# Optimization experiments

Hardware: AMD Instinct MI355X
Metric: run time of the kernel (lower is better)

Reference implementation:

```python
import jax, jax.numpy as jnp
import numpy as np

B, S, D, H = 4, 1024, 768, 12
DH = D // H  # 64
ALPHA = 0.5
EPS = 1e-12


def setup_inputs() -> dict:
    key = jax.random.key(0)
    ks = jax.random.split(key, 12)
    s = 0.02
    return {
        "hidden_states": jax.random.normal(ks[0], (B, S, D), jnp.float32),
        "attention_mask": jnp.zeros((B, 1, 1, S), jnp.float32),
        "previous_attention": jax.random.uniform(ks[1], (B, H, S, S), jnp.float32),
        "Wq": jax.random.normal(ks[2], (D, D), jnp.float32) * s,
        "bq": jnp.zeros((D,), jnp.float32),
        "Wk": jax.random.normal(ks[3], (D, D), jnp.float32) * s,
        "bk": jnp.zeros((D,), jnp.float32),
        "Wv": jax.random.normal(ks[4], (D, D), jnp.float32) * s,
        "bv": jnp.zeros((D,), jnp.float32),
        "conv_w": jax.random.normal(ks[5], (H, H), jnp.float32) * 0.1,  # 1x1 conv over head channels
        "conv_b": jnp.zeros((H,), jnp.float32),
        "Wo": jax.random.normal(ks[6], (D, D), jnp.float32) * s,
        "bo": jnp.zeros((D,), jnp.float32),
        "ln_w": jnp.ones((D,), jnp.float32),
        "ln_b": jnp.zeros((D,), jnp.float32),
    }


def _split_heads(x):
    # [B,S,D] -> [B,H,S,DH]
    return x.reshape(B, S, H, DH).transpose(0, 2, 1, 3)


def reference(hidden_states, attention_mask, previous_attention,
              Wq, bq, Wk, bk, Wv, bv, conv_w, conv_b, Wo, bo, ln_w, ln_b):
    q = _split_heads(hidden_states @ Wq + bq)
    k = _split_heads(hidden_states @ Wk + bk)
    v = _split_heads(hidden_states @ Wv + bv)

    scores = jnp.einsum('bhqd,bhkd->bhqk', q, k) / jnp.sqrt(jnp.float32(DH))
    scores = scores + attention_mask
    probs = jax.nn.softmax(scores, axis=-1)

    # 1x1 conv over head channels on previous attention, mix, re-softmax
    prev = jnp.einsum('oi,biqk->boqk', conv_w, previous_attention) + conv_b[None, :, None, None]
    probs = jax.nn.softmax(ALPHA * prev + (1.0 - ALPHA) * probs, axis=-1)

    ctx = jnp.einsum('bhqk,bhkd->bhqd', probs, v)
    ctx = ctx.transpose(0, 2, 1, 3).reshape(B, S, D)

    out = ctx @ Wo + bo
    out = out + hidden_states
    u = out.mean(-1, keepdims=True)
    var = ((out - u) ** 2).mean(-1, keepdims=True)
    out = (out - u) / jnp.sqrt(var + EPS)
    return ln_w * out + ln_b
```

## Files before the change

### kernel.cpp

```cpp
#include <hip/hip_runtime.h>
#include <math.h>

#define BB 4
#define SS 1024
#define DD 768
#define HH 12
#define DHH 64

typedef __attribute__((ext_vector_type(8))) short bf16x8;
typedef __attribute__((ext_vector_type(4))) float f32x4;

__device__ __forceinline__ unsigned int f2bf(float f) {
    unsigned int u = __float_as_uint(f);
    return (u + 0x7FFFu + ((u >> 16) & 1u)) >> 16;
}
__device__ __forceinline__ float bf2f(unsigned int h) {
    return __uint_as_float(h << 16);
}

__device__ __forceinline__ void glds16(const void* g, void* l) {
    __builtin_amdgcn_global_load_lds(
        (const __attribute__((address_space(1))) void*)g,
        (__attribute__((address_space(3))) void*)l, 16, 0, 0);
}

__global__ __launch_bounds__(256)
void cvt_hidden_kernel(const float* __restrict__ src, unsigned short* __restrict__ dst)
{
    const int idx = (blockIdx.x * 256 + threadIdx.x) * 8;
    float4 a = *(const float4*)&src[idx];
    float4 b = *(const float4*)&src[idx + 4];
    uint4 p;
    p.x = f2bf(a.x) | (f2bf(a.y) << 16);
    p.y = f2bf(a.z) | (f2bf(a.w) << 16);
    p.z = f2bf(b.x) | (f2bf(b.y) << 16);
    p.w = f2bf(b.z) | (f2bf(b.w) << 16);
    *(uint4*)&dst[idx] = p;
}

__global__ __launch_bounds__(256)
void transpose_w_kernel(const float* __restrict__ Wq, const float* __restrict__ Wk,
                        const float* __restrict__ Wv, const float* __restrict__ Wo,
                        unsigned short* __restrict__ Wt)
{
    __shared__ float tile[32][33];
    const int t = threadIdx.x;
    const int kt = blockIdx.x, nt = blockIdx.y, w = blockIdx.z;
    const float* src = (w == 0) ? Wq : (w == 1) ? Wk : (w == 2) ? Wv : Wo;
    const int r = t >> 3, c4 = (t & 7) * 4;
    float4 v = *(const float4*)&src[(kt * 32 + r) * DD + nt * 32 + c4];
    tile[r][c4 + 0] = v.x; tile[r][c4 + 1] = v.y;
    tile[r][c4 + 2] = v.z; tile[r][c4 + 3] = v.w;
    __syncthreads();
    uint2 p;
    p.x = f2bf(tile[c4 + 0][r]) | (f2bf(tile[c4 + 1][r]) << 16);
    p.y = f2bf(tile[c4 + 2][r]) | (f2bf(tile[c4 + 3][r]) << 16);
    *(uint2*)&Wt[((size_t)w * DD + nt * 32 + r) * DD + kt * 32 + c4] = p;
}

__device__ __forceinline__ void gemm_core64(
    const char* __restrict__ Ag, const char* __restrict__ Bg,
    char* As, char* Bs, int tid, f32x4 (&acc)[2][2])
{
    const int lane = tid & 63;
    const int wr = (tid >> 7) & 1;
    const int wc = (tid >> 6) & 1;
    const int ldst = (tid & 192) << 4;

    for (int c = 0; c < 12; ++c) {
        const int kbyte = c * 128;
        #pragma unroll
        for (int i = 0; i < 2; ++i) {
            const int s = i * 256 + tid;
            const int row = s >> 3, kb = s & 7;
            const size_t off = (size_t)row * 1536 + kbyte + ((kb ^ (row & 7)) << 4);
            glds16(Ag + off, As + i * 4096 + ldst);
            glds16(Bg + off, Bs + i * 4096 + ldst);
        }
        __syncthreads();
        #pragma unroll
        for (int ks = 0; ks < 2; ++ks) {
            const int kb = ks * 4 + (lane >> 4);
            bf16x8 a[2], b[2];
            #pragma unroll
            for (int mi = 0; mi < 2; ++mi) {
                const int row = wr * 32 + mi * 16 + (lane & 15);
                a[mi] = *(const bf16x8*)(As + row * 128 + ((kb ^ (row & 7)) << 4));
            }
            #pragma unroll
            for (int ni = 0; ni < 2; ++ni) {
                const int row = wc * 32 + ni * 16 + (lane & 15);
                b[ni] = *(const bf16x8*)(Bs + row * 128 + ((kb ^ (row & 7)) << 4));
            }
            #pragma unroll
            for (int mi = 0; mi < 2; ++mi)
                #pragma unroll
                for (int ni = 0; ni < 2; ++ni)
                    acc[mi][ni] = __builtin_amdgcn_mfma_f32_16x16x32_bf16(
                        a[mi], b[ni], acc[mi][ni], 0, 0, 0);
        }
        __syncthreads();
    }
}

__global__ __launch_bounds__(256)
void qkv_gemm_kernel(const unsigned short* __restrict__ hbf, const unsigned short* __restrict__ Wt,
                     const float* __restrict__ bq, const float* __restrict__ bk,
                     const float* __restrict__ bv,
                     unsigned short* __restrict__ Qb, unsigned short* __restrict__ Kb,
                     unsigned short* __restrict__ Vtb)
{
    __shared__ __align__(16) char As[8192];
    __shared__ __align__(16) char Bs[8192];
    const int tid = threadIdx.x;
    const int m0 = blockIdx.x * 64;
    const int w = blockIdx.y / 12;
    const int n0w = (blockIdx.y % 12) * 64;

    f32x4 acc[2][2];
    const f32x4 z4 = {0.f, 0.f, 0.f, 0.f};
    acc[0][0] = z4; acc[0][1] = z4; acc[1][0] = z4; acc[1][1] = z4;

    const char* Ag = (const char*)hbf + (size_t)m0 * 1536;
    const char* Bg = (const char*)Wt + ((size_t)w * DD + n0w) * 1536;
    gemm_core64(Ag, Bg, As, Bs, tid, acc);

    const int lane = tid & 63;
    const int wr = (tid >> 7) & 1, wc = (tid >> 6) & 1;
    const float* bias = (w == 0) ? bq : (w == 1) ? bk : bv;
    #pragma unroll
    for (int mi = 0; mi < 2; ++mi) {
        #pragma unroll
        for (int ni = 0; ni < 2; ++ni) {
            const int nw = n0w + wc * 32 + ni * 16 + (lane & 15);
            const int h = nw >> 6, d = nw & 63;
            const float bb = bias[nw];
            const int mrow = m0 + wr * 32 + mi * 16 + (lane >> 4) * 4;
            const int b = mrow >> 10, s = mrow & 1023;
            if (w == 2) {
                uint2 p;
                p.x = f2bf(acc[mi][ni][0] + bb) | (f2bf(acc[mi][ni][1] + bb) << 16);
                p.y = f2bf(acc[mi][ni][2] + bb) | (f2bf(acc[mi][ni][3] + bb) << 16);
                *(uint2*)&Vtb[(((size_t)b * HH + h) * DHH + d) * SS + s] = p;
            } else {
                unsigned short* dst = (w == 0) ? Qb : Kb;
                #pragma unroll
                for (int r = 0; r < 4; ++r)
                    dst[(((size_t)b * HH + h) * SS + (s + r)) * DHH + d] =
                        (unsigned short)f2bf(acc[mi][ni][r] + bb);
            }
        }
    }
}

__global__ __launch_bounds__(256)
void qk_exp_kernel(const unsigned short* __restrict__ Qb, const unsigned short* __restrict__ Kb,
                   const float* __restrict__ mask,
                   unsigned short* __restrict__ E1, float* __restrict__ Z1)
{
    __shared__ __align__(16) char Ks[32768];
    const int tid = threadIdx.x;
    const int lane = tid & 63;
    const int wv = tid >> 6;
    const int bh = blockIdx.x >> 4;
    const int q0 = (blockIdx.x & 15) * 64;
    const int b = bh / HH;
    const int qw = q0 + wv * 16;
    const int ldst = (tid & 192) << 4;

    const char* Qrow = (const char*)Qb + ((size_t)bh * SS + qw + (lane & 15)) * 128;
    bf16x8 aq0 = *(const bf16x8*)(Qrow + (lane >> 4) * 16);
    bf16x8 aq1 = *(const bf16x8*)(Qrow + 64 + (lane >> 4) * 16);

    float zr[4] = {0.f, 0.f, 0.f, 0.f};
    const char* Kbase = (const char*)Kb + (size_t)bh * SS * 128;

    for (int c = 0; c < 4; ++c) {
        #pragma unroll
        for (int i = 0; i < 8; ++i) {
            const int s = i * 256 + tid;
            const int row = s >> 3, kb = s & 7;
            glds16(Kbase + (size_t)(c * 256 + row) * 128 + ((kb ^ (row & 7)) << 4),
                   Ks + i * 4096 + ldst);
        }
        __syncthreads();
        #pragma unroll
        for (int nf = 0; nf < 16; ++nf) {
            const int krow = nf * 16 + (lane & 15);
            const int kx = krow & 7;
            bf16x8 b0 = *(const bf16x8*)(Ks + krow * 128 + (((lane >> 4) ^ kx) << 4));
            bf16x8 b1 = *(const bf16x8*)(Ks + krow * 128 + (((4 + (lane >> 4)) ^ kx) << 4));
            f32x4 accf = {0.f, 0.f, 0.f, 0.f};
            accf = __builtin_amdgcn_mfma_f32_16x16x32_bf16(aq0, b0, accf, 0, 0, 0);
            accf = __builtin_amdgcn_mfma_f32_16x16x32_bf16(aq1, b1, accf, 0, 0, 0);
            const int kcol = c * 256 + krow;
            const float mk = mask[b * SS + kcol];
            #pragma unroll
            for (int r = 0; r < 4; ++r) {
                const int q = qw + (lane >> 4) * 4 + r;
                const float e = __expf(accf[r] * 0.125f + mk);
                zr[r] += e;
                E1[((size_t)bh * SS + q) * SS + kcol] = (unsigned short)f2bf(e);
            }
        }
        __syncthreads();
    }

    #pragma unroll
    for (int r = 0; r < 4; ++r) {
        float z = zr[r];
        z += __shfl_xor(z, 1); z += __shfl_xor(z, 2);
        z += __shfl_xor(z, 4); z += __shfl_xor(z, 8);
        if ((lane & 15) == 0)
            Z1[(size_t)bh * SS + qw + (lane >> 4) * 4 + r] = z;
    }
}

__global__ __launch_bounds__(256)
void e2_kernel(unsigned short* __restrict__ E1, const float* __restrict__ Z1,
               const float* __restrict__ prev, const float* __restrict__ cw,
               const float* __restrict__ cb, float* __restrict__ Z2)
{
    __shared__ float cws[144], cbs[12], izs[12], zred[4][12];
    const int t = threadIdx.x;
    const int b = blockIdx.x >> 10;
    const int q = blockIdx.x & 1023;

    if (t < 144) cws[t] = cw[t];
    if (t < 12) {
        cbs[t] = cb[t];
        izs[t] = 1.0f / Z1[((size_t)(b * HH + t)) * SS + q];
    }
    __syncthreads();

    float z2[12];
    #pragma unroll
    for (int h = 0; h < 12; ++h) z2[h] = 0.f;

    #pragma unroll
    for (int c = 0; c < 2; ++c) {
        const int k = c * 512 + t * 2;
        float2 pv[12];
        #pragma unroll
        for (int i = 0; i < 12; ++i)
            pv[i] = *(const float2*)&prev[(((size_t)(b * HH + i)) * SS + q) * SS + k];
        const size_t e1base = (((size_t)(b * HH)) * SS + q) * SS + k;
        #pragma unroll
        for (int h = 0; h < 12; ++h) {
            float mix0 = cbs[h], mix1 = cbs[h];
            #pragma unroll
            for (int i = 0; i < 12; ++i) {
                mix0 = fmaf(cws[h * 12 + i], pv[i].x, mix0);
                mix1 = fmaf(cws[h * 12 + i], pv[i].y, mix1);
            }
            unsigned int u = *(unsigned int*)&E1[e1base + (size_t)h * SS * SS];
            const float p10 = bf2f(u & 0xFFFFu) * izs[h];
            const float p11 = bf2f(u >> 16) * izs[h];
            const float e0 = __expf(0.5f * (mix0 + p10));
            const float e1 = __expf(0.5f * (mix1 + p11));
            z2[h] += e0 + e1;
            *(unsigned int*)&E1[e1base + (size_t)h * SS * SS] = f2bf(e0) | (f2bf(e1) << 16);
        }
    }

    #pragma unroll
    for (int h = 0; h < 12; ++h) {
        float z = z2[h];
        for (int off = 32; off; off >>= 1) z += __shfl_xor(z, off);
        z2[h] = z;
    }
    if ((t & 63) == 0) {
        const int wv = t >> 6;
        #pragma unroll
        for (int h = 0; h < 12; ++h) zred[wv][h] = z2[h];
    }
    __syncthreads();
    if (t < 12)
        Z2[((size_t)(b * HH + t)) * SS + q] =
            zred[0][t] + zred[1][t] + zred[2][t] + zred[3][t];
}

__global__ __launch_bounds__(256)
void pv_kernel(const unsigned short* __restrict__ E2, const float* __restrict__ Z2,
               const unsigned short* __restrict__ Vtb, unsigned short* __restrict__ ctx)
{
    __shared__ __align__(16) char Es[8192];
    __shared__ __align__(16) char Vs[8192];
    const int tid = threadIdx.x;
    const int lane = tid & 63;
    const int wv = tid >> 6;
    const int bh = blockIdx.x >> 4;
    const int q0 = (blockIdx.x & 15) * 64;
    const int b = bh / HH, h = bh % HH;
    const int ldst = (tid & 192) << 4;

    f32x4 acc[4];
    const f32x4 z4 = {0.f, 0.f, 0.f, 0.f};
    acc[0] = z4; acc[1] = z4; acc[2] = z4; acc[3] = z4;

    const char* Ebase = (const char*)E2 + ((size_t)bh * SS + q0) * 2048;
    const char* Vbase = (const char*)Vtb + (size_t)bh * DHH * 2048;

    for (int c = 0; c < 16; ++c) {
        const int kbyte = c * 128;
        #pragma unroll
        for (int i = 0; i < 2; ++i) {
            const int s = i * 256 + tid;
            const int row = s >> 3, kb = s & 7;
            const size_t off = (size_t)row * 2048 + kbyte + ((kb ^ (row & 7)) << 4);
            glds16(Ebase + off, Es + i * 4096 + ldst);
            glds16(Vbase + off, Vs + i * 4096 + ldst);
        }
        __syncthreads();
        #pragma unroll
        for (int ks = 0; ks < 2; ++ks) {
            const int kb = ks * 4 + (lane >> 4);
            const int arow = wv * 16 + (lane & 15);
            bf16x8 a = *(const bf16x8*)(Es + arow * 128 + ((kb ^ (arow & 7)) << 4));
            #pragma unroll
            for (int nf = 0; nf < 4; ++nf) {
                const int vrow = nf * 16 + (lane & 15);
                bf16x8 bb = *(const bf16x8*)(Vs + vrow * 128 + ((kb ^ (vrow & 7)) << 4));
                acc[nf] = __builtin_amdgcn_mfma_f32_16x16x32_bf16(a, bb, acc[nf], 0, 0, 0);
            }
        }
        __syncthreads();
    }

    float iz[4];
    #pragma unroll
    for (int r = 0; r < 4; ++r)
        iz[r] = 1.0f / Z2[(size_t)bh * SS + q0 + wv * 16 + (lane >> 4) * 4 + r];

    #pragma unroll
    for (int nf = 0; nf < 4; ++nf) {
        const int d = nf * 16 + (lane & 15);
        #pragma unroll
        for (int r = 0; r < 4; ++r) {
            const int q = q0 + wv * 16 + (lane >> 4) * 4 + r;
            ctx[((size_t)(b * SS + q)) * DD + h * DHH + d] =
                (unsigned short)f2bf(acc[nf][r] * iz[r]);
        }
    }
}

__global__ __launch_bounds__(256)
void o_gemm_kernel(const unsigned short* __restrict__ ctx, const unsigned short* __restrict__ WtO,
                   const float* __restrict__ bo, float* __restrict__ gout)
{
    __shared__ __align__(16) char As[8192];
    __shared__ __align__(16) char Bs[8192];
    const int tid = threadIdx.x;
    const int m0 = blockIdx.x * 64;
    const int n0 = blockIdx.y * 64;

    f32x4 acc[2][2];
    const f32x4 z4 = {0.f, 0.f, 0.f, 0.f};
    acc[0][0] = z4; acc[0][1] = z4; acc[1][0] = z4; acc[1][1] = z4;

    gemm_core64((const char*)ctx + (size_t)m0 * 1536,
                (const char*)WtO + (size_t)n0 * 1536, As, Bs, tid, acc);

    const int lane = tid & 63;
    const int wr = (tid >> 7) & 1, wc = (tid >> 6) & 1;
    #pragma unroll
    for (int mi = 0; mi < 2; ++mi) {
        #pragma unroll
        for (int ni = 0; ni < 2; ++ni) {
            const int n = n0 + wc * 32 + ni * 16 + (lane & 15);
            const float bb = bo[n];
            const int mrow = m0 + wr * 32 + mi * 16 + (lane >> 4) * 4;
            #pragma unroll
            for (int r = 0; r < 4; ++r)
                gout[(size_t)(mrow + r) * DD + n] = acc[mi][ni][r] + bb;
        }
    }
}

__global__ __launch_bounds__(256)
void ln_kernel(const float* __restrict__ go, const float* __restrict__ hid,
               const float* __restrict__ lw, const float* __restrict__ lb,
               float* __restrict__ out)
{
    const int row = blockIdx.x;
    const int tid = threadIdx.x;
    const int lane = tid & 63, wave = tid >> 6;
    __shared__ float wsum[4], wsq[4];

    float x[3];
    float ssum = 0.f, ssq = 0.f;
    #pragma unroll
    for (int j = 0; j < 3; ++j) {
        const int n = tid + j * 256;
        const float v = go[(size_t)row * DD + n] + hid[(size_t)row * DD + n];
        x[j] = v; ssum += v; ssq += v * v;
    }
    for (int off = 32; off; off >>= 1) {
        ssum += __shfl_xor(ssum, off);
        ssq  += __shfl_xor(ssq, off);
    }
    if (lane == 0) { wsum[wave] = ssum; wsq[wave] = ssq; }
    __syncthreads();
    const float tsum = wsum[0] + wsum[1] + wsum[2] + wsum[3];
    const float tsq  = wsq[0] + wsq[1] + wsq[2] + wsq[3];
    const float mean = tsum * (1.0f / 768.0f);
    const float var  = tsq * (1.0f / 768.0f) - mean * mean;
    const float rstd = rsqrtf(var + 1e-12f);
    #pragma unroll
    for (int j = 0; j < 3; ++j) {
        const int n = tid + j * 256;
        out[(size_t)row * DD + n] = lw[n] * ((x[j] - mean) * rstd) + lb[n];
    }
}

extern "C" void kernel_launch(void* const* d_in, const int* in_sizes, int n_in,
                              void* d_out, int out_size, void* d_ws, size_t ws_size,
                              hipStream_t stream)
{
    const float* hidden = (const float*)d_in[0];
    const float* mask   = (const float*)d_in[1];
    const float* prev   = (const float*)d_in[2];
    const float* Wq = (const float*)d_in[3];  const float* bq = (const float*)d_in[4];
    const float* Wk = (const float*)d_in[5];  const float* bk = (const float*)d_in[6];
    const float* Wv = (const float*)d_in[7];  const float* bv = (const float*)d_in[8];
    const float* cw = (const float*)d_in[9];  const float* cb = (const float*)d_in[10];
    const float* Wo = (const float*)d_in[11]; const float* bo = (const float*)d_in[12];
    const float* lw = (const float*)d_in[13]; const float* lb = (const float*)d_in[14];
    float* out = (float*)d_out;

    char* w = (char*)d_ws;
    unsigned short* hbf = (unsigned short*)(w);
    unsigned short* Wt  = (unsigned short*)(w + 6291456);
    unsigned short* Qb  = (unsigned short*)(w + 11010048);
    unsigned short* Kb  = (unsigned short*)(w + 17301504);
    unsigned short* Vtb = (unsigned short*)(w + 23592960);
    unsigned short* E1  = (unsigned short*)(w + 29884416);
    float* Z1 = (float*)(w + 130547712);
    float* Z2 = (float*)(w + 130744320);
    unsigned short* ctx = hbf;
    float* gout = (float*)(w + 11010048);

    dim3 blk(256);
    cvt_hidden_kernel<<<dim3(1536), blk, 0, stream>>>(hidden, hbf);
    transpose_w_kernel<<<dim3(24, 24, 4), blk, 0, stream>>>(Wq, Wk, Wv, Wo, Wt);
    qkv_gemm_kernel<<<dim3(64, 36), blk, 0, stream>>>(hbf, Wt, bq, bk, bv, Qb, Kb, Vtb);
    qk_exp_kernel<<<dim3(768), blk, 0, stream>>>(Qb, Kb, mask, E1, Z1);
    e2_kernel<<<dim3(4096), blk, 0, stream>>>(E1, Z1, prev, cw, cb, Z2);
    pv_kernel<<<dim3(768), blk, 0, stream>>>(E1, Z2, Vtb, ctx);
    o_gemm_kernel<<<dim3(64, 12), blk, 0, stream>>>(ctx, Wt + (size_t)3 * DD * DD, bo, gout);
    ln_kernel<<<dim3(4096), blk, 0, stream>>>(gout, hidden, lw, lb, out);
}
```

Baseline: 464.8 us.

## Stage kernel epilogue outputs through swizzled LDS for coalesced vector stores

Four kernels (QKV GEMM, QK-exp, PV context, O GEMM) now write their MFMA accumulator fragments into an XOR-swizzled LDS tile and then emit wide 16-byte global stores, instead of scattered 2-byte or 4-byte stores. The biggest target is the E1 write of the B*H*S*S bf16 exponent matrix, which previously went out as strided 2-byte stores. This adds LDS traffic and extra __syncthreads per 64-column chunk in qk_exp, which may cut into overlap between compute and memory.

```diff
diff --git a/kernel.cpp b/kernel.cpp
--- a/kernel.cpp
+++ b/kernel.cpp
@@ -127,29 +127,53 @@
 
     const int lane = tid & 63;
     const int wr = (tid >> 7) & 1, wc = (tid >> 6) & 1;
+    const int b = m0 >> 10, s0 = m0 & 1023;
+    const int h = n0w >> 6;
     const float* bias = (w == 0) ? bq : (w == 1) ? bk : bv;
-    #pragma unroll
-    for (int mi = 0; mi < 2; ++mi) {
-        #pragma unroll
-        for (int ni = 0; ni < 2; ++ni) {
-            const int nw = n0w + wc * 32 + ni * 16 + (lane & 15);
-            const int h = nw >> 6, d = nw & 63;
-            const float bb = bias[nw];
-            const int mrow = m0 + wr * 32 + mi * 16 + (lane >> 4) * 4;
-            const int b = mrow >> 10, s = mrow & 1023;
-            if (w == 2) {
-                uint2 p;
-                p.x = f2bf(acc[mi][ni][0] + bb) | (f2bf(acc[mi][ni][1] + bb) << 16);
-                p.y = f2bf(acc[mi][ni][2] + bb) | (f2bf(acc[mi][ni][3] + bb) << 16);
-                *(uint2*)&Vtb[(((size_t)b * HH + h) * DHH + d) * SS + s] = p;
-            } else {
-                unsigned short* dst = (w == 0) ? Qb : Kb;
+
+    if (w == 2) {
+        #pragma unroll
+        for (int mi = 0; mi < 2; ++mi)
+            #pragma unroll
+            for (int ni = 0; ni < 2; ++ni) {
+                const int drow = wc * 32 + ni * 16 + (lane & 15);
+                const float bb = bias[n0w + drow];
                 #pragma unroll
-                for (int r = 0; r < 4; ++r)
-                    dst[(((size_t)b * HH + h) * SS + (s + r)) * DHH + d] =
-                        (unsigned short)f2bf(acc[mi][ni][r] + bb);
-            }
-        }
+                for (int r = 0; r < 4; ++r) {
+                    const int scol = wr * 32 + mi * 16 + (lane >> 4) * 4 + r;
+                    const int byte = (drow * 128 + scol * 2) ^ ((drow & 7) << 4);
+                    *(unsigned short*)(As + byte) = (unsigned short)f2bf(acc[mi][ni][r] + bb);
+                }
+            }
+        __syncthreads();
+        const int drow = tid >> 2, c32 = (tid & 3) * 32;
+        const int sw = (drow & 7) << 4;
+        uint4 lo = *(uint4*)(As + ((drow * 128 + c32) ^ sw));
+        uint4 hi = *(uint4*)(As + ((drow * 128 + c32 + 16) ^ sw));
+        char* dst = (char*)Vtb + ((((size_t)(b * HH + h) * DHH) + drow) * SS + s0) * 2 + c32;
+        *(uint4*)dst = lo; *(uint4*)(dst + 16) = hi;
+    } else {
+        #pragma unroll
+        for (int mi = 0; mi < 2; ++mi)
+            #pragma unroll
+            for (int ni = 0; ni < 2; ++ni) {
+                const int ncol = wc * 32 + ni * 16 + (lane & 15);
+                const float bb = bias[n0w + ncol];
+                #pragma unroll
+                for (int r = 0; r < 4; ++r) {
+                    const int srow = wr * 32 + mi * 16 + (lane >> 4) * 4 + r;
+                    const int byte = (srow * 128 + ncol * 2) ^ ((srow & 7) << 4);
+                    *(unsigned short*)(As + byte) = (unsigned short)f2bf(acc[mi][ni][r] + bb);
+                }
+            }
+        __syncthreads();
+        const int srow = tid >> 2, c32 = (tid & 3) * 32;
+        const int sw = (srow & 7) << 4;
+        uint4 lo = *(uint4*)(As + ((srow * 128 + c32) ^ sw));
+        uint4 hi = *(uint4*)(As + ((srow * 128 + c32 + 16) ^ sw));
+        unsigned short* base = (w == 0) ? Qb : Kb;
+        char* dst = (char*)base + (((size_t)(b * HH + h) * SS + s0 + srow) * DHH) * 2 + c32;
+        *(uint4*)dst = lo; *(uint4*)(dst + 16) = hi;
     }
 }
 
@@ -159,6 +183,7 @@
                    unsigned short* __restrict__ E1, float* __restrict__ Z1)
 {
     __shared__ __align__(16) char Ks[32768];
+    __shared__ __align__(16) char Es[8192];
     const int tid = threadIdx.x;
     const int lane = tid & 63;
     const int wv = tid >> 6;
@@ -184,26 +209,41 @@
                    Ks + i * 4096 + ldst);
         }
         __syncthreads();
-        #pragma unroll
-        for (int nf = 0; nf < 16; ++nf) {
-            const int krow = nf * 16 + (lane & 15);
-            const int kx = krow & 7;
-            bf16x8 b0 = *(const bf16x8*)(Ks + krow * 128 + (((lane >> 4) ^ kx) << 4));
-            bf16x8 b1 = *(const bf16x8*)(Ks + krow * 128 + (((4 + (lane >> 4)) ^ kx) << 4));
-            f32x4 accf = {0.f, 0.f, 0.f, 0.f};
-            accf = __builtin_amdgcn_mfma_f32_16x16x32_bf16(aq0, b0, accf, 0, 0, 0);
-            accf = __builtin_amdgcn_mfma_f32_16x16x32_bf16(aq1, b1, accf, 0, 0, 0);
-            const int kcol = c * 256 + krow;
-            const float mk = mask[b * SS + kcol];
-            #pragma unroll
-            for (int r = 0; r < 4; ++r) {
-                const int q = qw + (lane >> 4) * 4 + r;
-                const float e = __expf(accf[r] * 0.125f + mk);
-                zr[r] += e;
-                E1[((size_t)bh * SS + q) * SS + kcol] = (unsigned short)f2bf(e);
-            }
-        }
-        __syncthreads();
+        for (int kg = 0; kg < 4; ++kg) {
+            #pragma unroll
+            for (int nfi = 0; nfi < 4; ++nfi) {
+                const int nf = kg * 4 + nfi;
+                const int krow = nf * 16 + (lane & 15);
+                const int kx = krow & 7;
+                bf16x8 b0 = *(const bf16x8*)(Ks + krow * 128 + (((lane >> 4) ^ kx) << 4));
+                bf16x8 b1 = *(const bf16x8*)(Ks + krow * 128 + (((4 + (lane >> 4)) ^ kx) << 4));
+                f32x4 accf = {0.f, 0.f, 0.f, 0.f};
+                accf = __builtin_amdgcn_mfma_f32_16x16x32_bf16(aq0, b0, accf, 0, 0, 0);
+                accf = __builtin_amdgcn_mfma_f32_16x16x32_bf16(aq1, b1, accf, 0, 0, 0);
+                const int kcol = c * 256 + krow;
+                const float mk = mask[b * SS + kcol];
+                const int kl = nfi * 16 + (lane & 15);
+                #pragma unroll
+                for (int r = 0; r < 4; ++r) {
+                    const int ql = wv * 16 + (lane >> 4) * 4 + r;
+                    const float e = __expf(accf[r] * 0.125f + mk);
+                    zr[r] += e;
+                    const int byte = (ql * 128 + kl * 2) ^ ((ql & 7) << 4);
+                    *(unsigned short*)(Es + byte) = (unsigned short)f2bf(e);
+                }
+            }
+            __syncthreads();
+            {
+                const int ql = tid >> 2, c32 = (tid & 3) * 32;
+                const int sw = (ql & 7) << 4;
+                uint4 lo = *(uint4*)(Es + ((ql * 128 + c32) ^ sw));
+                uint4 hi = *(uint4*)(Es + ((ql * 128 + c32 + 16) ^ sw));
+                char* dst = (char*)E1 + ((size_t)bh * SS + q0 + ql) * 2048
+                          + (c * 256 + kg * 64) * 2 + c32;
+                *(uint4*)dst = lo; *(uint4*)(dst + 16) = hi;
+            }
+            __syncthreads();
+        }
     }
 
     #pragma unroll
@@ -337,10 +377,19 @@
         const int d = nf * 16 + (lane & 15);
         #pragma unroll
         for (int r = 0; r < 4; ++r) {
-            const int q = q0 + wv * 16 + (lane >> 4) * 4 + r;
-            ctx[((size_t)(b * SS + q)) * DD + h * DHH + d] =
-                (unsigned short)f2bf(acc[nf][r] * iz[r]);
-        }
+            const int ql = wv * 16 + (lane >> 4) * 4 + r;
+            const int byte = (ql * 128 + d * 2) ^ ((ql & 7) << 4);
+            *(unsigned short*)(Es + byte) = (unsigned short)f2bf(acc[nf][r] * iz[r]);
+        }
+    }
+    __syncthreads();
+    {
+        const int ql = tid >> 2, c32 = (tid & 3) * 32;
+        const int sw = (ql & 7) << 4;
+        uint4 lo = *(uint4*)(Es + ((ql * 128 + c32) ^ sw));
+        uint4 hi = *(uint4*)(Es + ((ql * 128 + c32 + 16) ^ sw));
+        char* dst = (char*)ctx + ((size_t)(b * SS + q0 + ql) * DD + h * DHH) * 2 + c32;
+        *(uint4*)dst = lo; *(uint4*)(dst + 16) = hi;
     }
 }
 
@@ -348,8 +397,9 @@
 void o_gemm_kernel(const unsigned short* __restrict__ ctx, const unsigned short* __restrict__ WtO,
                    const float* __restrict__ bo, float* __restrict__ gout)
 {
-    __shared__ __align__(16) char As[8192];
-    __shared__ __align__(16) char Bs[8192];
+    __shared__ __align__(16) char smem[16384];
+    char* As = smem;
+    char* Bs = smem + 8192;
     const int tid = threadIdx.x;
     const int m0 = blockIdx.x * 64;
     const int n0 = blockIdx.y * 64;
@@ -364,16 +414,30 @@
     const int lane = tid & 63;
     const int wr = (tid >> 7) & 1, wc = (tid >> 6) & 1;
     #pragma unroll
-    for (int mi = 0; mi < 2; ++mi) {
+    for (int mi = 0; mi < 2; ++mi)
         #pragma unroll
         for (int ni = 0; ni < 2; ++ni) {
-            const int n = n0 + wc * 32 + ni * 16 + (lane & 15);
-            const float bb = bo[n];
-            const int mrow = m0 + wr * 32 + mi * 16 + (lane >> 4) * 4;
-            #pragma unroll
-            for (int r = 0; r < 4; ++r)
-                gout[(size_t)(mrow + r) * DD + n] = acc[mi][ni][r] + bb;
-        }
+            const int ncol = wc * 32 + ni * 16 + (lane & 15);
+            const float bb = bo[n0 + ncol];
+            #pragma unroll
+            for (int r = 0; r < 4; ++r) {
+                const int row = wr * 32 + mi * 16 + (lane >> 4) * 4 + r;
+                *(float*)(smem + ((row * 256 + ncol * 4) ^ ((row & 7) << 4))) =
+                    acc[mi][ni][r] + bb;
+            }
+        }
+    __syncthreads();
+    {
+        const int row = tid >> 2, c64 = (tid & 3) * 64;
+        const int sw = (row & 7) << 4;
+        float4 v[4];
+        #pragma unroll
+        for (int j = 0; j < 4; ++j)
+            v[j] = *(float4*)(smem + ((row * 256 + c64 + j * 16) ^ sw));
+        float* dst = gout + (size_t)(m0 + row) * DD + n0 + (tid & 3) * 16;
+        #pragma unroll
+        for (int j = 0; j < 4; ++j)
+            *(float4*)(dst + j * 4) = v[j];
     }
 }
 
```

Result: no change. 468.8 us (+0.9%).
